# Kernel optimization log

Hardware: AMD Instinct MI355X
Metric: run time of the kernel (lower is better)

The kernel has to match this reference:

```python
import jax, jax.numpy as jnp
from jax import lax
import numpy as np

H, W = 4096, 4096
KERNEL_SIZES = [3, 5, 7, 9, 11, 13, 15]


def setup_inputs() -> dict:
    key = jax.random.key(0)
    k1, k2 = jax.random.split(key)
    x = jax.random.uniform(k1, (H, W), dtype=jnp.float32)
    base_map = jax.random.uniform(k2, (H, W), dtype=jnp.float32)
    return {"x": x, "base_map": base_map}


def _box_blur(x4, k):
    # replicate ('edge') padding by k//2, then VALID conv with uniform 1/k^2 kernel
    p = k // 2
    xp = jnp.pad(x4, ((0, 0), (0, 0), (p, p), (p, p)), mode='edge')
    w = jnp.full((1, 1, k, k), 1.0 / (k * k), dtype=x4.dtype)
    return lax.conv_general_dilated(
        xp, w, window_strides=(1, 1), padding='VALID',
        dimension_numbers=('NCHW', 'OIHW', 'NCHW'))


def reference(x, base_map):
    # x: [H, W] -> [1, 1, H, W]
    x4 = x[None, None, :, :]
    acc = jnp.zeros_like(x4)
    for k in KERNEL_SIZES:  # fixed small set of structurally distinct convs
        acc = acc + _box_blur(x4, k)
    out = (acc / len(KERNEL_SIZES)) * base_map[None, None, :, :]
    return out  # [1, 1, H, W]
```

## Files before the change

kernel.cpp:

```cpp
#include <hip/hip_runtime.h>

typedef __attribute__((ext_vector_type(2))) float f32x2;

#define W 4096
#define H 4096
#define NT 256
#define NW 4
#define COLS 512
#define SR 32
#define GROUP 4
#define NSTAGE (SR + 14)
#define NG 12
#define LW 576
#define RAD 7
#define PEND 18

__device__ __forceinline__ void gl_lds16(float* lds, const float* g) {
    __builtin_amdgcn_global_load_lds(
        (const __attribute__((address_space(1))) void*)g,
        (__attribute__((address_space(3))) void*)lds, 16, 0, 0);
}
__device__ __forceinline__ void gl_lds4(float* lds, const float* g) {
    __builtin_amdgcn_global_load_lds(
        (const __attribute__((address_space(1))) void*)g,
        (__attribute__((address_space(3))) void*)lds, 4, 0, 0);
}

__global__ __launch_bounds__(NT, 4) void multibox_kernel(
    const float* __restrict__ x, const float* __restrict__ base,
    float* __restrict__ out)
{
    __shared__ float buf[2][GROUP][LW];

    const int t  = threadIdx.x;
    const int w  = t >> 6;
    const int l  = t & 63;
    const int c0 = blockIdx.x * COLS;
    const int i0 = blockIdx.y * SR;

    const float w3  = 1.f/(7.f*9.f);
    const float w5  = 1.f/(7.f*25.f);
    const float w7  = 1.f/(7.f*49.f);
    const float w9  = 1.f/(7.f*81.f);
    const float w11 = 1.f/(7.f*121.f);
    const float w13 = 1.f/(7.f*169.f);
    const float w15 = 1.f/(7.f*225.f);

    const int colA = min(max(c0 -   8 + 4 * l, 0), W - 4);
    const int colB =         c0 + 248 + 4 * l;
    const int colC = min(    c0 + 504 +     l,     W - 1);

    auto stage = [&](int g, int b) {
        const int rc = min(max(i0 - RAD + g * GROUP + w, 0), H - 1);
        const float* rp = x + (size_t)rc * W;
        gl_lds16(&buf[b][w][0],   rp + colA);
        gl_lds16(&buf[b][w][256], rp + colB);
        gl_lds4 (&buf[b][w][512], rp + colC);
    };

    auto patch = [&](int b) {
        if (l < 8) buf[b][w][l] = buf[b][w][8];
    };

    f32x2 Pnd[PEND];
#pragma unroll
    for (int q = 0; q < PEND; ++q) Pnd[q] = f32x2{0.f, 0.f};

    auto compute_group = [&](int b, int g) {
#pragma unroll
        for (int rr = 0; rr < GROUP; ++rr) {
            if (g * GROUP + rr < NSTAGE) {
                const float* p = &buf[b][rr][2 * t];
                f32x2 q2[9];
#pragma unroll
                for (int i = 0; i < 9; ++i) q2[i] = *(const f32x2*)(p + 2 * i);

                auto PR = [&](int a) -> f32x2 {
                    if ((a & 1) == 0) return q2[a / 2];
                    f32x2 r;
                    r.x = q2[a / 2].y;
                    r.y = q2[a / 2 + 1].x;
                    return r;
                };

                f32x2 s3  = PR(7) + PR(8) + PR(9);
                f32x2 s5  = s3  + PR(6) + PR(10);
                f32x2 s7  = s5  + PR(5) + PR(11);
                f32x2 s9  = s7  + PR(4) + PR(12);
                f32x2 s11 = s9  + PR(3) + PR(13);
                f32x2 s13 = s11 + PR(2) + PR(14);
                f32x2 s15 = s13 + PR(1) + PR(15);

                f32x2 c7 = f32x2{w15, w15} * s15;
                f32x2 c6 = c7 + f32x2{w13, w13} * s13;
                f32x2 c5 = c6 + f32x2{w11, w11} * s11;
                f32x2 c4 = c5 + f32x2{w9 , w9 } * s9;
                f32x2 c3 = c4 + f32x2{w7 , w7 } * s7;
                f32x2 c2 = c3 + f32x2{w5 , w5 } * s5;
                f32x2 c1 = c2 + f32x2{w3 , w3 } * s3;

                Pnd[rr +  0] += c7; Pnd[rr +  1] += c6; Pnd[rr +  2] += c5;
                Pnd[rr +  3] += c4; Pnd[rr +  4] += c3; Pnd[rr +  5] += c2;
                Pnd[rr +  6] += c1; Pnd[rr +  7] += c1; Pnd[rr +  8] += c1;
                Pnd[rr +  9] += c2; Pnd[rr + 10] += c3; Pnd[rr + 11] += c4;
                Pnd[rr + 12] += c5; Pnd[rr + 13] += c6; Pnd[rr + 14] += c7;
            }
        }

#pragma unroll
        for (int p = 0; p < GROUP; ++p) {
            const int o_ofs = 4 * g - 14 + p;
            if (o_ofs >= 0 && o_ofs < SR) {
                const size_t bi = (size_t)(i0 + o_ofs) * W + c0 + 2 * t;
                f32x2 bm = *(const f32x2*)(base + bi);
                f32x2 ov = Pnd[p] * bm;
                *(f32x2*)(out + bi) = ov;
            }
        }

#pragma unroll
        for (int p = 0; p < PEND - GROUP; ++p) Pnd[p] = Pnd[p + GROUP];
#pragma unroll
        for (int p = PEND - GROUP; p < PEND; ++p) Pnd[p] = f32x2{0.f, 0.f};
    };

    stage(0, 0);
    __syncthreads();
    if (c0 == 0) { patch(0); __syncthreads(); }

#pragma clang loop unroll(disable)
    for (int g = 0; g < NG - 1; ++g) {
        stage(g + 1, (g + 1) & 1);
        compute_group(g & 1, g);
        __syncthreads();
        if (c0 == 0) { patch((g + 1) & 1); __syncthreads(); }
    }
    compute_group((NG - 1) & 1, NG - 1);
}

extern "C" void kernel_launch(void* const* d_in, const int* in_sizes, int n_in,
                              void* d_out, int out_size, void* d_ws, size_t ws_size,
                              hipStream_t stream) {
    const float* x    = (const float*)d_in[0];
    const float* base = (const float*)d_in[1];
    float* out        = (float*)d_out;

    dim3 grid(W / COLS, H / SR);
    multibox_kernel<<<grid, dim3(NT), 0, stream>>>(x, base, out);
}
```

Before: 45.91 us.

## Triple-buffer row staging with two-ahead prefetch and drop the edge-patch pass

Moves the LDS staging from double to triple buffering. Loads for group g+2 are issued while group g computes, and a manual s_waitcnt vmcnt plus a raw s_barrier replaces __syncthreads. The left halo is now fetched with per-lane clamped 4-byte loads, so replicate padding at the left image edge needs no separate patch step and no extra barrier. The cost is more LDS per block (27 KB instead of 18 KB), which could limit occupancy. The hand-counted vmcnt also depends on exactly four outstanding loads per wave per stage.

```diff
diff --git a/kernel.cpp b/kernel.cpp
--- a/kernel.cpp
+++ b/kernel.cpp
@@ -5,7 +5,6 @@
 #define W 4096
 #define H 4096
 #define NT 256
-#define NW 4
 #define COLS 512
 #define SR 32
 #define GROUP 4
@@ -30,7 +29,7 @@
     const float* __restrict__ x, const float* __restrict__ base,
     float* __restrict__ out)
 {
-    __shared__ float buf[2][GROUP][LW];
+    __shared__ float buf[3][GROUP][LW];
 
     const int t  = threadIdx.x;
     const int w  = t >> 6;
@@ -46,20 +45,19 @@
     const float w13 = 1.f/(7.f*169.f);
     const float w15 = 1.f/(7.f*225.f);
 
-    const int colA = min(max(c0 -   8 + 4 * l, 0), W - 4);
-    const int colB =         c0 + 248 + 4 * l;
-    const int colC = min(    c0 + 504 +     l,     W - 1);
+    const int colL  = min(max(c0 -   8 +     l, 0), W - 1);
+    const int colM1 =         c0 +  56 + 4 * l;
+    const int colM2 =         c0 + 312 + 4 * l;
+    const int colR  = min(    c0 + 504 +     l,     W - 1);
 
     auto stage = [&](int g, int b) {
         const int rc = min(max(i0 - RAD + g * GROUP + w, 0), H - 1);
         const float* rp = x + (size_t)rc * W;
-        gl_lds16(&buf[b][w][0],   rp + colA);
-        gl_lds16(&buf[b][w][256], rp + colB);
-        gl_lds4 (&buf[b][w][512], rp + colC);
-    };
-
-    auto patch = [&](int b) {
-        if (l < 8) buf[b][w][l] = buf[b][w][8];
+        float* lb = &buf[b][w][0];
+        gl_lds4 (lb,        rp + colL);
+        gl_lds16(lb +  64,  rp + colM1);
+        if (l < 48) gl_lds16(lb + 320, rp + colM2);
+        gl_lds4 (lb + 512,  rp + colR);
     };
 
     f32x2 Pnd[PEND];
@@ -125,17 +123,24 @@
     };
 
     stage(0, 0);
-    __syncthreads();
-    if (c0 == 0) { patch(0); __syncthreads(); }
+    stage(1, 1);
+    asm volatile("s_waitcnt vmcnt(4)" ::: "memory");
+    __builtin_amdgcn_s_barrier();
+    __builtin_amdgcn_sched_barrier(0);
 
+    int b = 0;
 #pragma clang loop unroll(disable)
-    for (int g = 0; g < NG - 1; ++g) {
-        stage(g + 1, (g + 1) & 1);
-        compute_group(g & 1, g);
-        __syncthreads();
-        if (c0 == 0) { patch((g + 1) & 1); __syncthreads(); }
+    for (int g = 0; g < NG; ++g) {
+        compute_group(b, g);
+        int b2 = b + 2; if (b2 >= 3) b2 -= 3;
+        if (g + 2 < NG) stage(g + 2, b2);
+        if (g + 1 < NG) {
+            asm volatile("s_waitcnt vmcnt(4)" ::: "memory");
+            __builtin_amdgcn_s_barrier();
+            __builtin_amdgcn_sched_barrier(0);
+        }
+        ++b; if (b >= 3) b = 0;
     }
-    compute_group((NG - 1) & 1, NG - 1);
 }
 
 extern "C" void kernel_launch(void* const* d_in, const int* in_sizes, int n_in,
```

Result: no change. 46.76 us (+1.9%).
